# Kernel tuning notes

Measured on AMD Instinct MI355X. Metric: run time of the kernel, lower is better.

Reference implementation:

```python
import jax, jax.numpy as jnp
import numpy as np
from jax import lax

B, T, H, L = 128, 512, 1024, 32


def setup_inputs() -> dict:
    key = jax.random.key(0)
    ks = jax.random.split(key, 8)
    outputs = jax.random.normal(ks[0], (B, T, H), jnp.float32)
    labels = jax.random.randint(ks[1], (B, T), 0, L)
    mask = jnp.ones((B, T), dtype=bool)
    fc_w = jax.random.normal(ks[2], (L, H), jnp.float32) * 0.02  # nn.Linear weight [out,in]
    fc_b = jnp.zeros((L,), jnp.float32)
    # torchcrf initializes transitions ~ U(-0.1, 0.1)
    start_transitions = jax.random.uniform(ks[3], (L,), jnp.float32, -0.1, 0.1)
    end_transitions = jax.random.uniform(ks[4], (L,), jnp.float32, -0.1, 0.1)
    transitions = jax.random.uniform(ks[5], (L, L), jnp.float32, -0.1, 0.1)
    return dict(outputs=outputs, labels=labels, mask=mask, fc_w=fc_w, fc_b=fc_b,
                start_transitions=start_transitions, end_transitions=end_transitions,
                transitions=transitions)


def reference(outputs, labels, mask, fc_w, fc_b, start_transitions, end_transitions, transitions):
    # emissions: [B, T, L]
    emissions = jnp.einsum('bth,lh->btl', outputs, fc_w) + fc_b
    b_, t_, l_ = emissions.shape
    mf = mask.astype(emissions.dtype)

    # ---- numerator: score of gold path (vectorized over time) ----
    first_tags = labels[:, 0]
    em_scores = jnp.take_along_axis(emissions, labels[..., None], axis=2)[..., 0]  # [B,T]
    trans_scores = transitions[labels[:, :-1], labels[:, 1:]]                       # [B,T-1]
    numerator = (start_transitions[first_tags] + em_scores[:, 0]
                 + jnp.sum((trans_scores + em_scores[:, 1:]) * mf[:, 1:], axis=1))
    seq_ends = mask.sum(axis=1).astype(jnp.int32) - 1
    last_tags = jnp.take_along_axis(labels, seq_ends[:, None], axis=1)[:, 0]
    numerator = numerator + end_transitions[last_tags]

    # ---- denominator: forward algorithm (logsumexp recurrence) ----
    score0 = start_transitions + emissions[:, 0]          # [B,L]
    em_rest = jnp.swapaxes(emissions[:, 1:], 0, 1)        # [T-1,B,L]
    m_rest = jnp.swapaxes(mask[:, 1:], 0, 1)              # [T-1,B]

    def fwd_step(score, xs):
        em_t, m_t = xs
        nxt = jax.nn.logsumexp(score[:, :, None] + transitions[None] + em_t[:, None, :], axis=1)
        return jnp.where(m_t[:, None], nxt, score), None

    score, _ = lax.scan(fwd_step, score0, (em_rest, m_rest))
    denominator = jax.nn.logsumexp(score + end_transitions, axis=1)

    llh = numerator - denominator
    loss = -jnp.mean(llh)  # reduction='mean', negated in the module

    # ---- Viterbi decode ----
    idx_l = jnp.arange(l_)

    def vit_step(score, xs):
        em_t, m_t = xs
        bcast = score[:, :, None] + transitions[None]     # [B,L_prev,L_next]
        nxt = bcast.max(axis=1) + em_t
        idx = jnp.argmax(bcast, axis=1)
        idx = jnp.where(m_t[:, None], idx, idx_l[None, :])  # identity pointer on padded steps
        return jnp.where(m_t[:, None], nxt, score), idx

    vscore, history = lax.scan(vit_step, score0, (em_rest, m_rest))  # history: [T-1,B,L]
    last_tag = jnp.argmax(vscore + end_transitions, axis=1)          # [B]

    def back_step(tag, idx):
        prev = jnp.take_along_axis(idx, tag[:, None], axis=1)[:, 0]
        return prev, prev

    _, prevs = lax.scan(back_step, last_tag, history, reverse=True)  # [T-1,B]
    pred = jnp.concatenate([prevs, last_tag[None]], axis=0).T        # [B,T]
    return loss, pred
```

## Files before the change

### kernel.cpp

```cpp
#include <hip/hip_runtime.h>

#define Bn 128
#define Tn 512
#define Hn 1024
#define Ln 32
#define L2E 1.44269504088896340736f
#define LN2 0.69314718055994530942f

#if __has_builtin(__builtin_amdgcn_exp2f)
#define EXP2F(x) __builtin_amdgcn_exp2f(x)
#else
#define EXP2F(x) exp2f(x)
#endif
#if __has_builtin(__builtin_amdgcn_logf)
#define LOG2F(x) __builtin_amdgcn_logf(x)
#else
#define LOG2F(x) log2f(x)
#endif

__device__ __forceinline__ float rfirstf(float v) {
  return __int_as_float(__builtin_amdgcn_readfirstlane(__float_as_int(v)));
}
__device__ __forceinline__ float bpermf(int byteidx, float v) {
  return __int_as_float(__builtin_amdgcn_ds_bpermute(byteidx, __float_as_int(v)));
}

#define DPPX(x, CTRL)                                                          \
  __int_as_float(__builtin_amdgcn_update_dpp(                                  \
      0, __float_as_int(x), (CTRL), 0xF, 0xF, false))

__device__ __forceinline__ float cross32f(float x, int l) {
#if __has_builtin(__builtin_amdgcn_permlane32_swap)
  int xi = __float_as_int(x);
  auto pp = __builtin_amdgcn_permlane32_swap(xi, xi, false, false);
  return __int_as_float(pp[0] ^ pp[1] ^ xi);
#else
  return __int_as_float(
      __builtin_amdgcn_ds_bpermute(((l ^ 32) << 2), __float_as_int(x)));
#endif
}

__device__ __forceinline__ int swap16i(int x) {
#if __has_builtin(__builtin_amdgcn_permlane16_swap)
  auto pp = __builtin_amdgcn_permlane16_swap(x, x, false, false);
  return pp[0] ^ pp[1] ^ x;
#else
  return __builtin_amdgcn_ds_swizzle(x, 0x401F);
#endif
}
__device__ __forceinline__ float swap16f(float x) {
  return __int_as_float(swap16i(__float_as_int(x)));
}

#define GATHER16(BASE, G)                                                      \
  float G##0 = (BASE);                                                         \
  float G##1 = DPPX(G##0, 0xB1);                                               \
  float G##2 = DPPX(G##0, 0x4E), G##3 = DPPX(G##1, 0x4E);                      \
  float G##4 = DPPX(G##3, 0x141), G##5 = DPPX(G##2, 0x141),                    \
        G##6 = DPPX(G##1, 0x141), G##7 = DPPX(G##0, 0x141);                    \
  float G##8 = DPPX(G##7, 0x140), G##9 = DPPX(G##6, 0x140),                    \
        G##10 = DPPX(G##5, 0x140), G##11 = DPPX(G##4, 0x140),                  \
        G##12 = DPPX(G##3, 0x140), G##13 = DPPX(G##2, 0x140),                  \
        G##14 = DPPX(G##1, 0x140), G##15 = DPPX(G##0, 0x140);

__global__ __launch_bounds__(512, 2) void k_emissions(
    const float* __restrict__ outs, const float* __restrict__ fcw,
    const float* __restrict__ fcb, float* __restrict__ emis,
    float* __restrict__ loss0)
{
  if (blockIdx.x == 0 && threadIdx.x == 0) loss0[0] = 0.0f;
  __shared__ float lw[32 * 1024];
  const int tid = threadIdx.x;

#pragma unroll
  for (int it = 0; it < 16; ++it) {
    int idx4 = it * 512 + tid;
    int j = idx4 >> 8;
    int kq = idx4 & 255;
    int sw = ((j >> 2) & 7) << 2;
    float4 v = *(const float4*)&fcw[(size_t)j * Hn + (kq << 2)];
    *(float4*)&lw[j * 1024 + ((kq << 2) ^ sw)] = v;
  }
  __syncthreads();

  const int jq = tid & 7;
  const int rg = tid >> 3;
  const int rowBase = blockIdx.x << 8;
  const float* xbase = outs + (size_t)(rowBase + rg * 4) * Hn;
  const int swr = jq << 2;
  const int j0 = jq << 2;

  float acc[4][4];
#pragma unroll
  for (int i = 0; i < 4; ++i)
#pragma unroll
    for (int jj = 0; jj < 4; ++jj) acc[i][jj] = 0.f;

  float4 xA[4][2], xB[4][2];
#pragma unroll
  for (int i = 0; i < 4; ++i) {
    xA[i][0] = *(const float4*)(xbase + i * Hn + 0);
    xA[i][1] = *(const float4*)(xbase + i * Hn + 4);
  }

#define EMI_LOAD(X, K0)                                                        \
  { _Pragma("unroll")                                                          \
    for (int i = 0; i < 4; ++i) {                                              \
      X[i][0] = *(const float4*)(xbase + i * Hn + (K0));                       \
      X[i][1] = *(const float4*)(xbase + i * Hn + (K0) + 4);                   \
    } }

#define EMI_COMP(X, K0)                                                        \
  { _Pragma("unroll")                                                          \
    for (int q = 0; q < 2; ++q) {                                              \
      const int kb = (K0) + q * 4;                                             \
      float4 w0 = *(const float4*)&lw[(j0 + 0) * 1024 + (kb ^ swr)];           \
      float4 w1 = *(const float4*)&lw[(j0 + 1) * 1024 + (kb ^ swr)];           \
      float4 w2r = *(const float4*)&lw[(j0 + 2) * 1024 + (kb ^ swr)];          \
      float4 w3r = *(const float4*)&lw[(j0 + 3) * 1024 + (kb ^ swr)];          \
      _Pragma("unroll")                                                        \
      for (int i = 0; i < 4; ++i) {                                            \
        float4 xv = X[i][q];                                                   \
        acc[i][0] = fmaf(xv.w, w0.w, fmaf(xv.z, w0.z,                          \
                    fmaf(xv.y, w0.y, fmaf(xv.x, w0.x, acc[i][0]))));           \
        acc[i][1] = fmaf(xv.w, w1.w, fmaf(xv.z, w1.z,                          \
                    fmaf(xv.y, w1.y, fmaf(xv.x, w1.x, acc[i][1]))));           \
        acc[i][2] = fmaf(xv.w, w2r.w, fmaf(xv.z, w2r.z,                        \
                    fmaf(xv.y, w2r.y, fmaf(xv.x, w2r.x, acc[i][2]))));         \
        acc[i][3] = fmaf(xv.w, w3r.w, fmaf(xv.z, w3r.z,                        \
                    fmaf(xv.y, w3r.y, fmaf(xv.x, w3r.x, acc[i][3]))));         \
      }                                                                        \
    } }

  for (int kc = 0; kc < 128; kc += 2) {
    EMI_LOAD(xB, (kc + 1) * 8)
    EMI_COMP(xA, kc * 8)
    if (kc + 2 < 128) EMI_LOAD(xA, (kc + 2) * 8)
    EMI_COMP(xB, (kc + 1) * 8)
  }
#undef EMI_LOAD
#undef EMI_COMP

  float bj[4];
#pragma unroll
  for (int jj = 0; jj < 4; ++jj) bj[jj] = fcb[j0 + jj];
#pragma unroll
  for (int i = 0; i < 4; ++i) {
    size_t row = (size_t)(rowBase + rg * 4 + i);
    float4 o = make_float4(acc[i][0] + bj[0], acc[i][1] + bj[1],
                           acc[i][2] + bj[2], acc[i][3] + bj[3]);
    *(float4*)&emis[row * 32 + j0] = o;
  }
}

__global__ __launch_bounds__(64) void k_scan(
    const float* __restrict__ emis, const int* __restrict__ labels,
    const float* __restrict__ trans, const float* __restrict__ startT,
    const float* __restrict__ endT, float* __restrict__ d_out)
{
  __shared__ int histI[512 * 32];
  __shared__ int hist2[256 * 32];
  __shared__ int hist4[128 * 32];
  __shared__ int tagsL[512];
  const int l = threadIdx.x;
  const int colc = (l & 15) | ((l & 32) >> 1);
  const int cb = colc ^ (l & 16);

  if (blockIdx.x < Bn) {
    const int b = blockIdx.x;
    const float* eb = emis + (size_t)b * Tn * Ln;

    float num = 0.f;
#pragma unroll
    for (int q = 0; q < 8; ++q) {
      int tt = l + q * 64;
      int lab = labels[b * Tn + tt];
      num += eb[tt * Ln + lab];
      if (tt > 0) num += trans[labels[b * Tn + tt - 1] * Ln + lab];
      if (tt == 0) num += startT[lab];
      if (tt == Tn - 1) num += endT[lab];
    }
#pragma unroll
    for (int m = 1; m < 64; m <<= 1) num += __shfl_xor(num, m, 64);

    float w[16];
#pragma unroll
    for (int m = 0; m < 16; ++m)
      w[m] = EXP2F(trans[(cb ^ m) * Ln + colc] * L2E);

    float p = 0.f, C2 = 0.f;
    for (int ww = 0; ww < 16; ++ww) {
      float emr[32];
#pragma unroll
      for (int tp = 0; tp < 32; ++tp)
        emr[tp] = eb[(ww * 32 + tp) * 32 + colc];
      if (ww == 0) {
        float v0 = (startT[colc] + emr[0]) * L2E;
        float a0i = rfirstf(v0);
        C2 = a0i;
        p = EXP2F(v0 - a0i);
      }
#pragma unroll
      for (int tp = 0; tp < 32; ++tp) {
        if (ww == 0 && tp == 0) continue;
        float crx = cross32f(p, l);
        float base = (l & 16) ? crx : p;
        GATHER16(base, gf)
        float A0 = fmaf(gf3, w[3], fmaf(gf2, w[2], fmaf(gf1, w[1], gf0 * w[0])));
        float A1 = fmaf(gf7, w[7], fmaf(gf6, w[6], fmaf(gf5, w[5], gf4 * w[4])));
        float A2 = fmaf(gf11, w[11], fmaf(gf10, w[10], fmaf(gf9, w[9], gf8 * w[8])));
        float A3 = fmaf(gf15, w[15], fmaf(gf14, w[14], fmaf(gf13, w[13], gf12 * w[12])));
        float Sh = (A0 + A1) + (A2 + A3);
        float S = Sh + swap16f(Sh);
        p = S * EXP2F(emr[tp] * L2E);
        if ((tp & 3) == 3) {
          int pb = __float_as_int(rfirstf(p));
          int ke = (pb >> 23) & 0xff;
          C2 += (float)(ke - 127);
          p *= __int_as_float((unsigned)(254 - ke) << 23);
        }
      }
    }
    float ex = p * EXP2F(endT[colc] * L2E);
#pragma unroll
    for (int m = 1; m < 64; m <<= 1) ex += __shfl_xor(ex, m, 64);
    float den = (C2 + LOG2F(ex) - 1.0f) * LN2;
    float llh = num - den;
    if (l == 0) atomicAdd(d_out, -llh * (1.0f / (float)Bn));
  } else {
    const int b = blockIdx.x - Bn;
    const float* eb = emis + (size_t)b * Tn * Ln;

    float t16[16];
#pragma unroll
    for (int m = 0; m < 16; ++m) t16[m] = trans[(cb ^ m) * Ln + colc];

    float r = 0.f;
    for (int ww = 0; ww < 16; ++ww) {
      float emr[32];
#pragma unroll
      for (int tp = 0; tp < 32; ++tp)
        emr[tp] = eb[(ww * 32 + tp) * 32 + colc];
      if (ww == 0) r = startT[colc] + emr[0];
#pragma unroll
      for (int tp = 0; tp < 32; ++tp) {
        if (ww == 0 && tp == 0) continue;
        float crx = cross32f(r, l);
        float base = (l & 16) ? crx : r;
        GATHER16(base, gv)
        float e0 = gv0 + t16[0], e1 = gv1 + t16[1], e2 = gv2 + t16[2],
              e3 = gv3 + t16[3], e4 = gv4 + t16[4], e5 = gv5 + t16[5],
              e6 = gv6 + t16[6], e7 = gv7 + t16[7], e8 = gv8 + t16[8],
              e9 = gv9 + t16[9], e10 = gv10 + t16[10], e11 = gv11 + t16[11],
              e12 = gv12 + t16[12], e13 = gv13 + t16[13], e14 = gv14 + t16[14],
              e15 = gv15 + t16[15];
        float m0 = fmaxf(fmaxf(e0, e1), e2);
        float m1 = fmaxf(fmaxf(e3, e4), e5);
        float m2 = fmaxf(fmaxf(e6, e7), e8);
        float m3 = fmaxf(fmaxf(e9, e10), e11);
        float m4 = fmaxf(fmaxf(e12, e13), e14);
        float Mh = fmaxf(fmaxf(fmaxf(m0, m1), m2),
                         fmaxf(fmaxf(m3, m4), e15));
        int amh = 15;
        amh = (e14 == Mh) ? 14 : amh;
        amh = (e13 == Mh) ? 13 : amh;
        amh = (e12 == Mh) ? 12 : amh;
        amh = (e11 == Mh) ? 11 : amh;
        amh = (e10 == Mh) ? 10 : amh;
        amh = (e9 == Mh) ? 9 : amh;
        amh = (e8 == Mh) ? 8 : amh;
        amh = (e7 == Mh) ? 7 : amh;
        amh = (e6 == Mh) ? 6 : amh;
        amh = (e5 == Mh) ? 5 : amh;
        amh = (e4 == Mh) ? 4 : amh;
        amh = (e3 == Mh) ? 3 : amh;
        amh = (e2 == Mh) ? 2 : amh;
        amh = (e1 == Mh) ? 1 : amh;
        amh = (e0 == Mh) ? 0 : amh;
        int srch = cb ^ amh;
        float Mo = swap16f(Mh);
        int srco = swap16i(srch);
        bool tk = (Mo > Mh) || (Mo == Mh && srco < srch);
        float M = tk ? Mo : Mh;
        int st = tk ? srco : srch;
        const int tm1 = ww * 32 + tp - 1;
        histI[tm1 * 32 + (colc ^ (tm1 & 31))] = st;
        r = M + emr[tp];
      }
    }

    float mv = r + endT[colc];
    int mi = colc;
#define RED_STEP(PAT)                                                          \
    {                                                                          \
      float ov2 = __int_as_float(__builtin_amdgcn_ds_swizzle(__float_as_int(mv), PAT)); \
      int oi2 = __builtin_amdgcn_ds_swizzle(mi, PAT);                          \
      bool take = (ov2 > mv) || (ov2 == mv && oi2 < mi);                       \
      mv = take ? ov2 : mv;                                                    \
      mi = take ? oi2 : mi;                                                    \
    }
    RED_STEP(0x401F) RED_STEP(0x201F) RED_STEP(0x101F) RED_STEP(0x081F) RED_STEP(0x041F)
#undef RED_STEP
    {
      float ovx = bpermf((l ^ 32) << 2, mv);
      int oix = __builtin_amdgcn_ds_bpermute((l ^ 32) << 2, mi);
      bool take = (ovx > mv) || (ovx == mv && oix < mi);
      mv = take ? ovx : mv;
      mi = take ? oix : mi;
    }
    const int lastTag = mi;
    __syncthreads();

    for (int e = l; e < 255 * 32; e += 64) {
      int t2 = e >> 5, jx = e & 31, t = t2 << 1;
      int a = histI[(t + 1) * 32 + (jx ^ ((t + 1) & 31))];
      int bb = histI[t * 32 + (a ^ (t & 31))];
      hist2[t2 * 32 + (jx ^ (t2 & 31))] = bb;
    }
    __syncthreads();
    for (int e = l; e < 127 * 32; e += 64) {
      int t4 = e >> 5, jx = e & 31;
      int a = hist2[(2 * t4 + 1) * 32 + (jx ^ ((2 * t4 + 1) & 31))];
      int bb = hist2[(2 * t4) * 32 + (a ^ ((2 * t4) & 31))];
      hist4[t4 * 32 + (jx ^ (t4 & 31))] = bb;
    }
    __syncthreads();

    int tag = lastTag;
    if (l == 0) tagsL[511] = tag;
    tag = histI[510 * 32 + (tag ^ (510 & 31))];
    if (l == 0) tagsL[510] = tag;
    int cur = hist2[254 * 32 + (tag ^ (254 & 31))];
    if (l == 0) tagsL[508] = cur;
    for (int t4 = 126; t4 >= 0; --t4) {
      cur = hist4[t4 * 32 + (cur ^ (t4 & 31))];
      if (l == 0) tagsL[t4 << 2] = cur;
    }
    __syncthreads();
    for (int e = l; e < 127; e += 64) {
      int t2 = 2 * e + 1, t = t2 << 1;
      int tp2 = tagsL[t + 2];
      tagsL[t] = hist2[t2 * 32 + (tp2 ^ (t2 & 31))];
    }
    __syncthreads();
    for (int e = l; e < 255; e += 64) {
      int t = 2 * e + 1;
      int tp1 = tagsL[t + 1];
      tagsL[t] = histI[t * 32 + (tp1 ^ (t & 31))];
    }
    __syncthreads();

    float* predf = d_out + 1 + (size_t)b * Tn;
#pragma unroll
    for (int q = 0; q < 8; ++q) {
      int t = q * 64 + l;
      predf[t] = (float)tagsL[t];
    }
  }
}

extern "C" void kernel_launch(void* const* d_in, const int* in_sizes, int n_in,
                              void* d_out, int out_size, void* d_ws, size_t ws_size,
                              hipStream_t stream) {
  const float* outs = (const float*)d_in[0];
  const int* labels = (const int*)d_in[1];
  const float* fcw = (const float*)d_in[3];
  const float* fcb = (const float*)d_in[4];
  const float* stT = (const float*)d_in[5];
  const float* enT = (const float*)d_in[6];
  const float* trn = (const float*)d_in[7];
  float* emis = (float*)d_ws;
  float* out = (float*)d_out;

  hipLaunchKernelGGL(k_emissions, dim3(256), dim3(512), 0, stream,
                     outs, fcw, fcb, emis, out);
  hipLaunchKernelGGL(k_scan, dim3(256), dim3(64), 0, stream,
                     emis, labels, trn, stT, enT, out);
}
```

Baseline: 245.5 us.

## Overlap second half of emission GEMM with CRF scans using flags, bf16 weights

The emission projection is split in two. The first kernel computes the first half of each sequence's timesteps. A second merged kernel computes the remaining half while scan blocks start the forward and Viterbi recurrences, spinning on per-chunk global flags before they need the later emissions. FC weights are staged in LDS as bf16, halving LDS use so more blocks fit. The Viterbi history is stored as bytes, and the pointer-doubling backtrace uses 512 threads. The risks are spin-wait deadlock if scan blocks get scheduled before the producers, and the reduced precision of the bf16 weights.

```diff
diff --git a/kernel.cpp b/kernel.cpp
--- a/kernel.cpp
+++ b/kernel.cpp
@@ -6,6 +6,9 @@
 #define Ln 32
 #define L2E 1.44269504088896340736f
 #define LN2 0.69314718055994530942f
+
+typedef unsigned char uchar;
+typedef unsigned short ushort_t;
 
 #if __has_builtin(__builtin_amdgcn_exp2f)
 #define EXP2F(x) __builtin_amdgcn_exp2f(x)
@@ -18,6 +21,8 @@
 #define LOG2F(x) log2f(x)
 #endif
 
+__device__ int g_flags[256];
+
 __device__ __forceinline__ float rfirstf(float v) {
   return __int_as_float(__builtin_amdgcn_readfirstlane(__float_as_int(v)));
 }
@@ -39,7 +44,6 @@
       __builtin_amdgcn_ds_bpermute(((l ^ 32) << 2), __float_as_int(x)));
 #endif
 }
-
 __device__ __forceinline__ int swap16i(int x) {
 #if __has_builtin(__builtin_amdgcn_permlane16_swap)
   auto pp = __builtin_amdgcn_permlane16_swap(x, x, false, false);
@@ -63,49 +67,55 @@
         G##12 = DPPX(G##3, 0x140), G##13 = DPPX(G##2, 0x140),                  \
         G##14 = DPPX(G##1, 0x140), G##15 = DPPX(G##0, 0x140);
 
-__global__ __launch_bounds__(512, 2) void k_emissions(
-    const float* __restrict__ outs, const float* __restrict__ fcw,
-    const float* __restrict__ fcb, float* __restrict__ emis,
-    float* __restrict__ loss0)
-{
-  if (blockIdx.x == 0 && threadIdx.x == 0) loss0[0] = 0.0f;
-  __shared__ float lw[32 * 1024];
-  const int tid = threadIdx.x;
-
+__device__ __forceinline__ ushort_t f2bf(float f) {
+  unsigned int x = __float_as_uint(f);
+  unsigned int r = x + 0x7FFFu + ((x >> 16) & 1u);
+  return (ushort_t)(r >> 16);
+}
+__device__ __forceinline__ float bf2f(ushort_t u) {
+  return __uint_as_float(((unsigned int)u) << 16);
+}
+
+__device__ __forceinline__ void stage_w_bf16(const float* __restrict__ fcw,
+                                             ushort_t* lwu, int tid) {
 #pragma unroll
   for (int it = 0; it < 16; ++it) {
     int idx4 = it * 512 + tid;
     int j = idx4 >> 8;
     int kq = idx4 & 255;
-    int sw = ((j >> 2) & 7) << 2;
     float4 v = *(const float4*)&fcw[(size_t)j * Hn + (kq << 2)];
-    *(float4*)&lw[j * 1024 + ((kq << 2) ^ sw)] = v;
-  }
-  __syncthreads();
-
+    ushort4 u;
+    u.x = f2bf(v.x); u.y = f2bf(v.y); u.z = f2bf(v.z); u.w = f2bf(v.w);
+    *(ushort4*)&lwu[j * 1024 + ((kq << 2) ^ ((j & 7) << 3))] = u;
+  }
+}
+
+__device__ __forceinline__ void em_rows128(
+    const float* __restrict__ outs, const float* __restrict__ fcb,
+    float* __restrict__ emis, const ushort_t* lwu, int rowBase, int tid)
+{
   const int jq = tid & 7;
   const int rg = tid >> 3;
-  const int rowBase = blockIdx.x << 8;
-  const float* xbase = outs + (size_t)(rowBase + rg * 4) * Hn;
-  const int swr = jq << 2;
   const int j0 = jq << 2;
-
-  float acc[4][4];
-#pragma unroll
-  for (int i = 0; i < 4; ++i)
+  const float* xbase = outs + (size_t)(rowBase + rg * 2) * Hn;
+  const int swb = (jq & 1) << 5;
+
+  float acc[2][4];
+#pragma unroll
+  for (int i = 0; i < 2; ++i)
 #pragma unroll
     for (int jj = 0; jj < 4; ++jj) acc[i][jj] = 0.f;
 
-  float4 xA[4][2], xB[4][2];
-#pragma unroll
-  for (int i = 0; i < 4; ++i) {
+  float4 xA[2][2], xB[2][2];
+#pragma unroll
+  for (int i = 0; i < 2; ++i) {
     xA[i][0] = *(const float4*)(xbase + i * Hn + 0);
     xA[i][1] = *(const float4*)(xbase + i * Hn + 4);
   }
 
 #define EMI_LOAD(X, K0)                                                        \
   { _Pragma("unroll")                                                          \
-    for (int i = 0; i < 4; ++i) {                                              \
+    for (int i = 0; i < 2; ++i) {                                              \
       X[i][0] = *(const float4*)(xbase + i * Hn + (K0));                       \
       X[i][1] = *(const float4*)(xbase + i * Hn + (K0) + 4);                   \
     } }
@@ -114,21 +124,25 @@
   { _Pragma("unroll")                                                          \
     for (int q = 0; q < 2; ++q) {                                              \
       const int kb = (K0) + q * 4;                                             \
-      float4 w0 = *(const float4*)&lw[(j0 + 0) * 1024 + (kb ^ swr)];           \
-      float4 w1 = *(const float4*)&lw[(j0 + 1) * 1024 + (kb ^ swr)];           \
-      float4 w2r = *(const float4*)&lw[(j0 + 2) * 1024 + (kb ^ swr)];          \
-      float4 w3r = *(const float4*)&lw[(j0 + 3) * 1024 + (kb ^ swr)];          \
+      ushort4 u0 = *(const ushort4*)&lwu[(j0 + 0) * 1024 + (kb ^ (swb | 0))];  \
+      ushort4 u1 = *(const ushort4*)&lwu[(j0 + 1) * 1024 + (kb ^ (swb | 8))];  \
+      ushort4 u2 = *(const ushort4*)&lwu[(j0 + 2) * 1024 + (kb ^ (swb | 16))]; \
+      ushort4 u3 = *(const ushort4*)&lwu[(j0 + 3) * 1024 + (kb ^ (swb | 24))]; \
+      float w0x = bf2f(u0.x), w0y = bf2f(u0.y), w0z = bf2f(u0.z), w0w = bf2f(u0.w); \
+      float w1x = bf2f(u1.x), w1y = bf2f(u1.y), w1z = bf2f(u1.z), w1w = bf2f(u1.w); \
+      float w2x = bf2f(u2.x), w2y = bf2f(u2.y), w2z = bf2f(u2.z), w2w = bf2f(u2.w); \
+      float w3x = bf2f(u3.x), w3y = bf2f(u3.y), w3z = bf2f(u3.z), w3w = bf2f(u3.w); \
       _Pragma("unroll")                                                        \
-      for (int i = 0; i < 4; ++i) {                                            \
+      for (int i = 0; i < 2; ++i) {                                            \
         float4 xv = X[i][q];                                                   \
-        acc[i][0] = fmaf(xv.w, w0.w, fmaf(xv.z, w0.z,                          \
-                    fmaf(xv.y, w0.y, fmaf(xv.x, w0.x, acc[i][0]))));           \
-        acc[i][1] = fmaf(xv.w, w1.w, fmaf(xv.z, w1.z,                          \
-                    fmaf(xv.y, w1.y, fmaf(xv.x, w1.x, acc[i][1]))));           \
-        acc[i][2] = fmaf(xv.w, w2r.w, fmaf(xv.z, w2r.z,                        \
-                    fmaf(xv.y, w2r.y, fmaf(xv.x, w2r.x, acc[i][2]))));         \
-        acc[i][3] = fmaf(xv.w, w3r.w, fmaf(xv.z, w3r.z,                        \
-                    fmaf(xv.y, w3r.y, fmaf(xv.x, w3r.x, acc[i][3]))));         \
+        acc[i][0] = fmaf(xv.w, w0w, fmaf(xv.z, w0z,                            \
+                    fmaf(xv.y, w0y, fmaf(xv.x, w0x, acc[i][0]))));             \
+        acc[i][1] = fmaf(xv.w, w1w, fmaf(xv.z, w1z,                            \
+                    fmaf(xv.y, w1y, fmaf(xv.x, w1x, acc[i][1]))));             \
+        acc[i][2] = fmaf(xv.w, w2w, fmaf(xv.z, w2z,                            \
+                    fmaf(xv.y, w2y, fmaf(xv.x, w2x, acc[i][2]))));             \
+        acc[i][3] = fmaf(xv.w, w3w, fmaf(xv.z, w3z,                            \
+                    fmaf(xv.y, w3y, fmaf(xv.x, w3x, acc[i][3]))));             \
       }                                                                        \
     } }
 
@@ -141,47 +155,75 @@
 #undef EMI_LOAD
 #undef EMI_COMP
 
-  float bj[4];
-#pragma unroll
-  for (int jj = 0; jj < 4; ++jj) bj[jj] = fcb[j0 + jj];
-#pragma unroll
-  for (int i = 0; i < 4; ++i) {
-    size_t row = (size_t)(rowBase + rg * 4 + i);
-    float4 o = make_float4(acc[i][0] + bj[0], acc[i][1] + bj[1],
-                           acc[i][2] + bj[2], acc[i][3] + bj[3]);
+  float b0 = fcb[j0], b1 = fcb[j0 + 1], b2 = fcb[j0 + 2], b3 = fcb[j0 + 3];
+#pragma unroll
+  for (int i = 0; i < 2; ++i) {
+    size_t row = (size_t)(rowBase + rg * 2 + i);
+    float4 o = make_float4(acc[i][0] + b0, acc[i][1] + b1,
+                           acc[i][2] + b2, acc[i][3] + b3);
     *(float4*)&emis[row * 32 + j0] = o;
   }
 }
 
-__global__ __launch_bounds__(64) void k_scan(
-    const float* __restrict__ emis, const int* __restrict__ labels,
-    const float* __restrict__ trans, const float* __restrict__ startT,
-    const float* __restrict__ endT, float* __restrict__ d_out)
+__global__ __launch_bounds__(512, 4) void k_em1(
+    const float* __restrict__ outs, const float* __restrict__ fcw,
+    const float* __restrict__ fcb, float* __restrict__ emis,
+    float* __restrict__ d_out)
 {
-  __shared__ int histI[512 * 32];
-  __shared__ int hist2[256 * 32];
-  __shared__ int hist4[128 * 32];
-  __shared__ int tagsL[512];
-  const int l = threadIdx.x;
-  const int colc = (l & 15) | ((l & 32) >> 1);
-  const int cb = colc ^ (l & 16);
-
-  if (blockIdx.x < Bn) {
-    const int b = blockIdx.x;
+  const int tid = threadIdx.x;
+  if (blockIdx.x == 0) {
+    if (tid < 256) g_flags[tid] = 0;
+    else if (tid == 256) d_out[0] = 0.f;
+  }
+  __shared__ ushort_t lwu[32768];
+  stage_w_bf16(fcw, lwu, tid);
+  __syncthreads();
+  const int seq = blockIdx.x >> 1, half = blockIdx.x & 1;
+  em_rows128(outs, fcb, emis, lwu, seq * 512 + half * 128, tid);
+}
+
+__global__ __launch_bounds__(512, 4) void k2(
+    const float* __restrict__ outs, const float* __restrict__ fcw,
+    const float* __restrict__ fcb, float* __restrict__ emis,
+    const int* __restrict__ labels, const float* __restrict__ trans,
+    const float* __restrict__ startT, const float* __restrict__ endT,
+    float* __restrict__ d_out)
+{
+  __shared__ __align__(16) char ldsU[65536];
+  const int tid = threadIdx.x;
+  const int g = blockIdx.x;
+
+  if (g < 256) {
+    ushort_t* lwu = (ushort_t*)ldsU;
+    stage_w_bf16(fcw, lwu, tid);
+    __syncthreads();
+    const int seq = g >> 1, half = g & 1;
+    em_rows128(outs, fcb, emis, lwu, seq * 512 + 256 + half * 128, tid);
+    __syncthreads();
+    if (tid == 0) {
+      __threadfence();
+      __hip_atomic_store(&g_flags[seq * 2 + half], 1, __ATOMIC_RELEASE,
+                         __HIP_MEMORY_SCOPE_AGENT);
+    }
+    return;
+  }
+
+#define WAITF(IDX)                                                             \
+  {                                                                            \
+    while (__hip_atomic_load(&g_flags[IDX], __ATOMIC_ACQUIRE,                  \
+                             __HIP_MEMORY_SCOPE_AGENT) == 0)                   \
+      __builtin_amdgcn_s_sleep(8);                                             \
+    __threadfence();                                                           \
+  }
+
+  const int s = g - 256;
+  if (s < 128) {
+    if (tid >= 64) return;
+    const int l = tid;
+    const int colc = (l & 15) | ((l & 32) >> 1);
+    const int cb = colc ^ (l & 16);
+    const int b = s;
     const float* eb = emis + (size_t)b * Tn * Ln;
-
-    float num = 0.f;
-#pragma unroll
-    for (int q = 0; q < 8; ++q) {
-      int tt = l + q * 64;
-      int lab = labels[b * Tn + tt];
-      num += eb[tt * Ln + lab];
-      if (tt > 0) num += trans[labels[b * Tn + tt - 1] * Ln + lab];
-      if (tt == 0) num += startT[lab];
-      if (tt == Tn - 1) num += endT[lab];
-    }
-#pragma unroll
-    for (int m = 1; m < 64; m <<= 1) num += __shfl_xor(num, m, 64);
 
     float w[16];
 #pragma unroll
@@ -190,6 +232,8 @@
 
     float p = 0.f, C2 = 0.f;
     for (int ww = 0; ww < 16; ++ww) {
+      if (ww == 8) WAITF(b * 2)
+      if (ww == 12) WAITF(b * 2 + 1)
       float emr[32];
 #pragma unroll
       for (int tp = 0; tp < 32; ++tp)
@@ -221,6 +265,20 @@
         }
       }
     }
+
+    float num = 0.f;
+#pragma unroll
+    for (int q = 0; q < 8; ++q) {
+      int tt = l + q * 64;
+      int lab = labels[b * Tn + tt];
+      num += eb[tt * Ln + lab];
+      if (tt > 0) num += trans[labels[b * Tn + tt - 1] * Ln + lab];
+      if (tt == 0) num += startT[lab];
+      if (tt == Tn - 1) num += endT[lab];
+    }
+#pragma unroll
+    for (int m = 1; m < 64; m <<= 1) num += __shfl_xor(num, m, 64);
+
     float ex = p * EXP2F(endT[colc] * L2E);
 #pragma unroll
     for (int m = 1; m < 64; m <<= 1) ex += __shfl_xor(ex, m, 64);
@@ -228,135 +286,147 @@
     float llh = num - den;
     if (l == 0) atomicAdd(d_out, -llh * (1.0f / (float)Bn));
   } else {
-    const int b = blockIdx.x - Bn;
+    const int b = s - 128;
+    uchar* h1 = (uchar*)ldsU;
+    uchar* h2 = (uchar*)ldsU + 16384;
+    uchar* h4 = (uchar*)ldsU + 24576;
+    int* tagsL = (int*)(ldsU + 28672);
     const float* eb = emis + (size_t)b * Tn * Ln;
 
-    float t16[16];
-#pragma unroll
-    for (int m = 0; m < 16; ++m) t16[m] = trans[(cb ^ m) * Ln + colc];
-
-    float r = 0.f;
-    for (int ww = 0; ww < 16; ++ww) {
-      float emr[32];
-#pragma unroll
-      for (int tp = 0; tp < 32; ++tp)
-        emr[tp] = eb[(ww * 32 + tp) * 32 + colc];
-      if (ww == 0) r = startT[colc] + emr[0];
-#pragma unroll
-      for (int tp = 0; tp < 32; ++tp) {
-        if (ww == 0 && tp == 0) continue;
-        float crx = cross32f(r, l);
-        float base = (l & 16) ? crx : r;
-        GATHER16(base, gv)
-        float e0 = gv0 + t16[0], e1 = gv1 + t16[1], e2 = gv2 + t16[2],
-              e3 = gv3 + t16[3], e4 = gv4 + t16[4], e5 = gv5 + t16[5],
-              e6 = gv6 + t16[6], e7 = gv7 + t16[7], e8 = gv8 + t16[8],
-              e9 = gv9 + t16[9], e10 = gv10 + t16[10], e11 = gv11 + t16[11],
-              e12 = gv12 + t16[12], e13 = gv13 + t16[13], e14 = gv14 + t16[14],
-              e15 = gv15 + t16[15];
-        float m0 = fmaxf(fmaxf(e0, e1), e2);
-        float m1 = fmaxf(fmaxf(e3, e4), e5);
-        float m2 = fmaxf(fmaxf(e6, e7), e8);
-        float m3 = fmaxf(fmaxf(e9, e10), e11);
-        float m4 = fmaxf(fmaxf(e12, e13), e14);
-        float Mh = fmaxf(fmaxf(fmaxf(m0, m1), m2),
-                         fmaxf(fmaxf(m3, m4), e15));
-        int amh = 15;
-        amh = (e14 == Mh) ? 14 : amh;
-        amh = (e13 == Mh) ? 13 : amh;
-        amh = (e12 == Mh) ? 12 : amh;
-        amh = (e11 == Mh) ? 11 : amh;
-        amh = (e10 == Mh) ? 10 : amh;
-        amh = (e9 == Mh) ? 9 : amh;
-        amh = (e8 == Mh) ? 8 : amh;
-        amh = (e7 == Mh) ? 7 : amh;
-        amh = (e6 == Mh) ? 6 : amh;
-        amh = (e5 == Mh) ? 5 : amh;
-        amh = (e4 == Mh) ? 4 : amh;
-        amh = (e3 == Mh) ? 3 : amh;
-        amh = (e2 == Mh) ? 2 : amh;
-        amh = (e1 == Mh) ? 1 : amh;
-        amh = (e0 == Mh) ? 0 : amh;
-        int srch = cb ^ amh;
-        float Mo = swap16f(Mh);
-        int srco = swap16i(srch);
-        bool tk = (Mo > Mh) || (Mo == Mh && srco < srch);
-        float M = tk ? Mo : Mh;
-        int st = tk ? srco : srch;
-        const int tm1 = ww * 32 + tp - 1;
-        histI[tm1 * 32 + (colc ^ (tm1 & 31))] = st;
-        r = M + emr[tp];
+    if (tid < 64) {
+      const int l = tid;
+      const int colc = (l & 15) | ((l & 32) >> 1);
+      const int cb = colc ^ (l & 16);
+
+      float t16[16];
+#pragma unroll
+      for (int m = 0; m < 16; ++m) t16[m] = trans[(cb ^ m) * Ln + colc];
+
+      float r = 0.f;
+      for (int ww = 0; ww < 16; ++ww) {
+        if (ww == 8) WAITF(b * 2)
+        if (ww == 12) WAITF(b * 2 + 1)
+        float emr[32];
+#pragma unroll
+        for (int tp = 0; tp < 32; ++tp)
+          emr[tp] = eb[(ww * 32 + tp) * 32 + colc];
+        if (ww == 0) r = startT[colc] + emr[0];
+#pragma unroll
+        for (int tp = 0; tp < 32; ++tp) {
+          if (ww == 0 && tp == 0) continue;
+          float crx = cross32f(r, l);
+          float base = (l & 16) ? crx : r;
+          GATHER16(base, gv)
+          float e0 = gv0 + t16[0], e1 = gv1 + t16[1], e2 = gv2 + t16[2],
+                e3 = gv3 + t16[3], e4 = gv4 + t16[4], e5 = gv5 + t16[5],
+                e6 = gv6 + t16[6], e7 = gv7 + t16[7], e8 = gv8 + t16[8],
+                e9 = gv9 + t16[9], e10 = gv10 + t16[10], e11 = gv11 + t16[11],
+                e12 = gv12 + t16[12], e13 = gv13 + t16[13], e14 = gv14 + t16[14],
+                e15 = gv15 + t16[15];
+          float m0 = fmaxf(fmaxf(e0, e1), e2);
+          float m1 = fmaxf(fmaxf(e3, e4), e5);
+          float m2 = fmaxf(fmaxf(e6, e7), e8);
+          float m3 = fmaxf(fmaxf(e9, e10), e11);
+          float m4 = fmaxf(fmaxf(e12, e13), e14);
+          float Mh = fmaxf(fmaxf(fmaxf(m0, m1), m2),
+                           fmaxf(fmaxf(m3, m4), e15));
+          int amh = 15;
+          amh = (e14 == Mh) ? 14 : amh;
+          amh = (e13 == Mh) ? 13 : amh;
+          amh = (e12 == Mh) ? 12 : amh;
+          amh = (e11 == Mh) ? 11 : amh;
+          amh = (e10 == Mh) ? 10 : amh;
+          amh = (e9 == Mh) ? 9 : amh;
+          amh = (e8 == Mh) ? 8 : amh;
+          amh = (e7 == Mh) ? 7 : amh;
+          amh = (e6 == Mh) ? 6 : amh;
+          amh = (e5 == Mh) ? 5 : amh;
+          amh = (e4 == Mh) ? 4 : amh;
+          amh = (e3 == Mh) ? 3 : amh;
+          amh = (e2 == Mh) ? 2 : amh;
+          amh = (e1 == Mh) ? 1 : amh;
+          amh = (e0 == Mh) ? 0 : amh;
+          int srch = cb ^ amh;
+          float Mo = swap16f(Mh);
+          int srco = swap16i(srch);
+          bool tk = (Mo > Mh) || (Mo == Mh && srco < srch);
+          float M = tk ? Mo : Mh;
+          int st = tk ? srco : srch;
+          const int tm1 = ww * 32 + tp - 1;
+          h1[tm1 * 32 + (colc ^ (tm1 & 31))] = (uchar)st;
+          r = M + emr[tp];
+        }
       }
-    }
-
-    float mv = r + endT[colc];
-    int mi = colc;
+
+      float mv = r + endT[colc];
+      int mi = colc;
 #define RED_STEP(PAT)                                                          \
-    {                                                                          \
-      float ov2 = __int_as_float(__builtin_amdgcn_ds_swizzle(__float_as_int(mv), PAT)); \
-      int oi2 = __builtin_amdgcn_ds_swizzle(mi, PAT);                          \
-      bool take = (ov2 > mv) || (ov2 == mv && oi2 < mi);                       \
-      mv = take ? ov2 : mv;                                                    \
-      mi = take ? oi2 : mi;                                                    \
-    }
-    RED_STEP(0x401F) RED_STEP(0x201F) RED_STEP(0x101F) RED_STEP(0x081F) RED_STEP(0x041F)
+      {                                                                        \
+        float ov2 = __int_as_float(__builtin_amdgcn_ds_swizzle(__float_as_int(mv), PAT)); \
+        int oi2 = __builtin_amdgcn_ds_swizzle(mi, PAT);                        \
+        bool take = (ov2 > mv) || (ov2 == mv && oi2 < mi);                     \
+        mv = take ? ov2 : mv;                                                  \
+        mi = take ? oi2 : mi;                                                  \
+      }
+      RED_STEP(0x401F) RED_STEP(0x201F) RED_STEP(0x101F) RED_STEP(0x081F) RED_STEP(0x041F)
 #undef RED_STEP
-    {
-      float ovx = bpermf((l ^ 32) << 2, mv);
-      int oix = __builtin_amdgcn_ds_bpermute((l ^ 32) << 2, mi);
-      bool take = (ovx > mv) || (ovx == mv && oix < mi);
-      mv = take ? ovx : mv;
-      mi = take ? oix : mi;
-    }
-    const int lastTag = mi;
-    __syncthreads();
-
-    for (int e = l; e < 255 * 32; e += 64) {
+      {
+        float ovx = bpermf((l ^ 32) << 2, mv);
+        int oix = __builtin_amdgcn_ds_bpermute((l ^ 32) << 2, mi);
+        bool take = (ovx > mv) || (ovx == mv && oix < mi);
+        mv = take ? ovx : mv;
+        mi = take ? oix : mi;
+      }
+      if (tid == 0) tagsL[511] = mi;
+    }
+    __syncthreads();
+    const int lastTag = tagsL[511];
+
+#pragma unroll 4
+    for (int e = tid; e < 255 * 32; e += 512) {
       int t2 = e >> 5, jx = e & 31, t = t2 << 1;
-      int a = histI[(t + 1) * 32 + (jx ^ ((t + 1) & 31))];
-      int bb = histI[t * 32 + (a ^ (t & 31))];
-      hist2[t2 * 32 + (jx ^ (t2 & 31))] = bb;
-    }
-    __syncthreads();
-    for (int e = l; e < 127 * 32; e += 64) {
+      int a = h1[(t + 1) * 32 + (jx ^ ((t + 1) & 31))];
+      int bb = h1[t * 32 + (a ^ (t & 31))];
+      h2[t2 * 32 + (jx ^ (t2 & 31))] = (uchar)bb;
+    }
+    __syncthreads();
+#pragma unroll 4
+    for (int e = tid; e < 127 * 32; e += 512) {
       int t4 = e >> 5, jx = e & 31;
-      int a = hist2[(2 * t4 + 1) * 32 + (jx ^ ((2 * t4 + 1) & 31))];
-      int bb = hist2[(2 * t4) * 32 + (a ^ ((2 * t4) & 31))];
-      hist4[t4 * 32 + (jx ^ (t4 & 31))] = bb;
+      int a = h2[(2 * t4 + 1) * 32 + (jx ^ ((2 * t4 + 1) & 31))];
+      int bb = h2[(2 * t4) * 32 + (a ^ ((2 * t4) & 31))];
+      h4[t4 * 32 + (jx ^ (t4 & 31))] = (uchar)bb;
     }
     __syncthreads();
 
     int tag = lastTag;
-    if (l == 0) tagsL[511] = tag;
-    tag = histI[510 * 32 + (tag ^ (510 & 31))];
-    if (l == 0) tagsL[510] = tag;
-    int cur = hist2[254 * 32 + (tag ^ (254 & 31))];
-    if (l == 0) tagsL[508] = cur;
+    if (tid == 0) tagsL[511] = tag;
+    tag = h1[510 * 32 + (tag ^ (510 & 31))];
+    if (tid == 0) tagsL[510] = tag;
+    int cur = h2[254 * 32 + (tag ^ (254 & 31))];
+    if (tid == 0) tagsL[508] = cur;
     for (int t4 = 126; t4 >= 0; --t4) {
-      cur = hist4[t4 * 32 + (cur ^ (t4 & 31))];
-      if (l == 0) tagsL[t4 << 2] = cur;
-    }
-    __syncthreads();
-    for (int e = l; e < 127; e += 64) {
+      cur = h4[t4 * 32 + (cur ^ (t4 & 31))];
+      if (tid == 0) tagsL[t4 << 2] = cur;
+    }
+    __syncthreads();
+    for (int e = tid; e < 127; e += 512) {
       int t2 = 2 * e + 1, t = t2 << 1;
       int tp2 = tagsL[t + 2];
-      tagsL[t] = hist2[t2 * 32 + (tp2 ^ (t2 & 31))];
-    }
-    __syncthreads();
-    for (int e = l; e < 255; e += 64) {
+      tagsL[t] = h2[t2 * 32 + (tp2 ^ (t2 & 31))];
+    }
+    __syncthreads();
+    for (int e = tid; e < 255; e += 512) {
       int t = 2 * e + 1;
       int tp1 = tagsL[t + 1];
-      tagsL[t] = histI[t * 32 + (tp1 ^ (t & 31))];
+      tagsL[t] = h1[t * 32 + (tp1 ^ (t & 31))];
     }
     __syncthreads();
 
     float* predf = d_out + 1 + (size_t)b * Tn;
-#pragma unroll
-    for (int q = 0; q < 8; ++q) {
-      int t = q * 64 + l;
-      predf[t] = (float)tagsL[t];
-    }
-  }
+    predf[tid] = (float)tagsL[tid];
+  }
+#undef WAITF
 }
 
 extern "C" void kernel_launch(void* const* d_in, const int* in_sizes, int n_in,
@@ -372,8 +442,8 @@
   float* emis = (float*)d_ws;
   float* out = (float*)d_out;
 
-  hipLaunchKernelGGL(k_emissions, dim3(256), dim3(512), 0, stream,
+  hipLaunchKernelGGL(k_em1, dim3(256), dim3(512), 0, stream,
                      outs, fcw, fcb, emis, out);
-  hipLaunchKernelGGL(k_scan, dim3(256), dim3(64), 0, stream,
-                     emis, labels, trn, stT, enT, out);
-}
+  hipLaunchKernelGGL(k2, dim3(512), dim3(512), 0, stream,
+                     outs, fcw, fcb, emis, labels, trn, stT, enT, out);
+}
```

Result: slower. 253.8 us (+3.4%).
